# Performance work log

Hardware: AMD Instinct MI355X
Metric: run time of the kernel (lower is better)

The kernel has to match this reference:

```python
import jax, jax.numpy as jnp
import numpy as np

D = 512
EPS = 1e-5  # torch BatchNorm1d default eps


def swish(x):
    return x * jax.nn.sigmoid(x)


def batchnorm_train(x, gamma, beta):
    # BatchNorm1d in training mode: biased batch stats
    m = jnp.mean(x, axis=0)
    v = jnp.mean((x - m) ** 2, axis=0)
    return gamma * (x - m) / jnp.sqrt(v + EPS) + beta


def setup_inputs() -> dict:
    key = jax.random.key(0)
    k_fea, k_w1, k_w2, k_lerp = jax.random.split(key, 4)
    bs, P = 32768, 8192
    fea = jax.random.normal(k_fea, (bs, D), dtype=jnp.float32)
    # first P rows are the minority (positive) class
    lbl = jnp.concatenate([jnp.ones((P, 1), jnp.int32), jnp.zeros((bs - P, 1), jnp.int32)], axis=0)
    scale = 1.0 / np.sqrt(D)
    W1 = jax.random.normal(k_w1, (D, D), dtype=jnp.float32) * scale
    W2 = jax.random.normal(k_w2, (D, D), dtype=jnp.float32) * scale
    b1 = jnp.zeros((D,), jnp.float32)
    b2 = jnp.zeros((D,), jnp.float32)
    g1 = jnp.ones((D,), jnp.float32)
    g2 = jnp.ones((D,), jnp.float32)
    beta1 = jnp.zeros((D,), jnp.float32)
    beta2 = jnp.zeros((D,), jnp.float32)
    lerp_w = jax.random.uniform(k_lerp, (P, 3), dtype=jnp.float32)
    return dict(fea=fea, lbl=lbl, W1=W1, b1=b1, g1=g1, beta1=beta1,
                W2=W2, b2=b2, g2=g2, beta2=beta2, lerp_w=lerp_w, num_pos=P)


def reference(fea, lbl, W1, b1, g1, beta1, W2, b2, g2, beta2, lerp_w, num_pos):
    # fea_transform: Linear -> BN -> Swish -> Linear -> BN -> Swish
    h = swish(batchnorm_train(fea @ W1 + b1, g1, beta1))
    h = swish(batchnorm_train(h @ W2 + b2, g2, beta2))

    # SMOTE path (training mode): KNN over positive-class features
    pos_idx = jnp.nonzero(lbl[:, 0] > 0, size=num_pos)[0]  # static-size gather
    x = h[pos_idx]                                          # (P, D)
    sq = jnp.sum(x * x, axis=-1)                            # (P,)
    # negative squared pairwise distance; topk largest == nearest
    neg_dist = 2.0 * (x @ x.T) - sq[:, None] - sq[None, :]  # (P, P)
    _, idx = jax.lax.top_k(neg_dist, 3)                     # (P, 3), idx[:,0] == self

    a = x[idx[:, 0]]                                        # (P, D) anchor
    b = x[idx]                                              # (P, 3, D) neighbors
    # torch.lerp(a, b, w) = a + w * (b - a), one random w per (i, j)
    new_fea = a[:, None, :] + lerp_w[..., None] * (b - a[:, None, :])
    new_fea = new_fea.reshape(-1, D)                        # (3P, D), row-major matches i,j loop order

    fea_out = jnp.concatenate([h, new_fea], axis=0)
    lbl_out = jnp.concatenate([lbl, jnp.ones((new_fea.shape[0], 1), lbl.dtype)], axis=0)
    return fea_out, lbl_out
```

## Files before the change

### kernel.cpp

```cpp
#include <hip/hip_runtime.h>
#include <math.h>

#define NEG_INF -3.402823466e38f

typedef __attribute__((ext_vector_type(8))) short bf16x8;
typedef __attribute__((ext_vector_type(4))) float f32x4;

__device__ __forceinline__ void gload_lds16(const unsigned short* g, unsigned short* l) {
  __builtin_amdgcn_global_load_lds(
      (const __attribute__((address_space(1))) unsigned int*)g,
      (__attribute__((address_space(3))) unsigned int*)l, 16, 0, 0);
}
__device__ __forceinline__ void gload_lds16f(const float* g, float* l) {
  __builtin_amdgcn_global_load_lds(
      (const __attribute__((address_space(1))) unsigned int*)g,
      (__attribute__((address_space(3))) unsigned int*)l, 16, 0, 0);
}

__device__ __forceinline__ unsigned short f2bf(float f) {
  union { float f; unsigned int u; } a; a.f = f;
  unsigned int u = a.u;
  return (unsigned short)((u + 0x7fffu + ((u >> 16) & 1u)) >> 16);
}

__device__ __forceinline__ void split3_8(f32x4 a, f32x4 b,
                                         bf16x8& hi, bf16x8& md, bf16x8& lo) {
  union { bf16x8 v; unsigned int u[4]; } H, M, L;
  float f[8];
  f[0]=a[0]; f[1]=a[1]; f[2]=a[2]; f[3]=a[3];
  f[4]=b[0]; f[5]=b[1]; f[6]=b[2]; f[7]=b[3];
#pragma unroll
  for (int p = 0; p < 4; ++p) {
    union { float f; unsigned int u; } x0, x1, h0, h1, r0, r1, m0, m1, s0, s1;
    x0.f = f[2*p]; x1.f = f[2*p+1];
    H.u[p] = (x0.u >> 16) | (x1.u & 0xffff0000u);
    h0.u = x0.u & 0xffff0000u; h1.u = x1.u & 0xffff0000u;
    r0.f = x0.f - h0.f;        r1.f = x1.f - h1.f;
    M.u[p] = (r0.u >> 16) | (r1.u & 0xffff0000u);
    m0.u = r0.u & 0xffff0000u; m1.u = r1.u & 0xffff0000u;
    s0.f = r0.f - m0.f;        s1.f = r1.f - m1.f;
    L.u[p] = (s0.u >> 16) | (s1.u & 0xffff0000u);
  }
  hi = H.v; md = M.v; lo = L.v;
}

__global__ __launch_bounds__(256) void split_w_t3(const float* __restrict__ W,
    unsigned short* __restrict__ Th, unsigned short* __restrict__ Tm,
    unsigned short* __restrict__ Tl)
{
  __shared__ float T[64][65];
  int k0 = blockIdx.x * 64, n0 = blockIdx.y * 64;
  int tid = threadIdx.x;
  int r = tid >> 4, c4 = (tid & 15) << 2;
#pragma unroll
  for (int p = 0; p < 4; ++p) {
    int row = r + p * 16;
    float4 v = *(const float4*)&W[(size_t)(k0 + row) * 512 + n0 + c4];
    T[c4 + 0][row] = v.x; T[c4 + 1][row] = v.y;
    T[c4 + 2][row] = v.z; T[c4 + 3][row] = v.w;
  }
  __syncthreads();
  int nr = tid >> 2, kc = (tid & 3) << 4;
#pragma unroll
  for (int u = 0; u < 16; ++u) {
    union { float f; unsigned int u; } x, h, rr, m, ss;
    x.f = T[nr][kc + u];
    unsigned short hb = (unsigned short)(x.u >> 16);
    h.u = x.u & 0xffff0000u;
    rr.f = x.f - h.f;
    unsigned short mb = (unsigned short)(rr.u >> 16);
    m.u = rr.u & 0xffff0000u;
    ss.f = rr.f - m.f;
    unsigned short lb = (unsigned short)(ss.u >> 16);
    size_t o = (size_t)(n0 + nr) * 512 + k0 + kc + u;
    Th[o] = hb; Tm[o] = mb; Tl[o] = lb;
  }
}

__global__ __launch_bounds__(256, 2) void gemm_split3(
    const float* __restrict__ A, const unsigned short* __restrict__ Bth,
    const unsigned short* __restrict__ Btm, const unsigned short* __restrict__ Btl,
    const float* __restrict__ bias, float* __restrict__ C, float* __restrict__ partial)
{
  __shared__ char smem[81920];
  const int tid = threadIdx.x;
  const int w = tid >> 6, lane = tid & 63;
  const int bm = blockIdx.x * 128, bn = blockIdx.y * 128;
  const int fr = lane & 15, fg = lane >> 4;
  const int arow = tid >> 3, acb = (tid & 7) << 4;
  const int brow = tid >> 2, bcb = (tid & 3) << 4;

  f32x4 acc[2][8];
#pragma unroll
  for (int mi = 0; mi < 2; ++mi)
#pragma unroll
    for (int ni = 0; ni < 8; ++ni) acc[mi][ni] = (f32x4){0.f, 0.f, 0.f, 0.f};

  auto STAGE = [&](int buf, int ktf) {
    float* sA = (float*)(smem + buf * 40960);
    unsigned short* sBh = (unsigned short*)(smem + buf * 40960 + 16384);
    unsigned short* sBm = sBh + 4096;
    unsigned short* sBl = sBm + 4096;
#pragma unroll
    for (int p = 0; p < 4; ++p) {
      int row = arow + p * 32;
      int cb = acb ^ ((row & 7) << 4);
      gload_lds16f(&A[(size_t)(bm + row) * 512 + ktf + (cb >> 2)],
                   &sA[row * 32 + (acb >> 2)]);
    }
#pragma unroll
    for (int p = 0; p < 2; ++p) {
      int row = brow + p * 64;
      int cb = bcb ^ (((row >> 1) & 3) << 4);
      int so = row * 32 + (bcb >> 1);
      gload_lds16(&Bth[(size_t)(bn + row) * 512 + ktf + (cb >> 1)], &sBh[so]);
      gload_lds16(&Btm[(size_t)(bn + row) * 512 + ktf + (cb >> 1)], &sBm[so]);
      gload_lds16(&Btl[(size_t)(bn + row) * 512 + ktf + (cb >> 1)], &sBl[so]);
    }
  };

  STAGE(0, 0);
  __syncthreads();
  for (int it = 0; it < 16; ++it) {
    int cur = it & 1;
    if (it + 1 < 16) STAGE(cur ^ 1, (it + 1) * 32);
    float* sA = (float*)(smem + cur * 40960);
    unsigned short* sBh = (unsigned short*)(smem + cur * 40960 + 16384);
    unsigned short* sBm = sBh + 4096;
    unsigned short* sBl = sBm + 4096;
    bf16x8 ah[2], am[2], al[2];
#pragma unroll
    for (int mi = 0; mi < 2; ++mi) {
      int row = w * 32 + mi * 16 + fr;
      int swz = (row & 7) << 4;
      const char* rb = (const char*)(sA + row * 32);
      f32x4 f0 = *(const f32x4*)(rb + ((fg * 32) ^ swz));
      f32x4 f1 = *(const f32x4*)(rb + ((fg * 32 + 16) ^ swz));
      split3_8(f0, f1, ah[mi], am[mi], al[mi]);
    }
#pragma unroll
    for (int ni = 0; ni < 8; ++ni) {
      int row = ni * 16 + fr;
      int off = row * 32 + (((fg * 16) ^ (((row >> 1) & 3) << 4)) >> 1);
      bf16x8 bh  = *(const bf16x8*)&sBh[off];
      bf16x8 bmf = *(const bf16x8*)&sBm[off];
      bf16x8 blf = *(const bf16x8*)&sBl[off];
#pragma unroll
      for (int mi = 0; mi < 2; ++mi) {
        acc[mi][ni] = __builtin_amdgcn_mfma_f32_16x16x32_bf16(al[mi], bh,  acc[mi][ni], 0, 0, 0);
        acc[mi][ni] = __builtin_amdgcn_mfma_f32_16x16x32_bf16(am[mi], bmf, acc[mi][ni], 0, 0, 0);
        acc[mi][ni] = __builtin_amdgcn_mfma_f32_16x16x32_bf16(ah[mi], blf, acc[mi][ni], 0, 0, 0);
        acc[mi][ni] = __builtin_amdgcn_mfma_f32_16x16x32_bf16(am[mi], bh,  acc[mi][ni], 0, 0, 0);
        acc[mi][ni] = __builtin_amdgcn_mfma_f32_16x16x32_bf16(ah[mi], bmf, acc[mi][ni], 0, 0, 0);
        acc[mi][ni] = __builtin_amdgcn_mfma_f32_16x16x32_bf16(ah[mi], bh,  acc[mi][ni], 0, 0, 0);
      }
    }
    __syncthreads();
  }

  float ssv[8], qqv[8];
#pragma unroll
  for (int ni = 0; ni < 8; ++ni) {
    float bno = bias[bn + ni * 16 + fr];
    float s = 0.f, q = 0.f;
#pragma unroll
    for (int mi = 0; mi < 2; ++mi) {
      int row = bm + w * 32 + mi * 16 + fg * 4;
      int col = bn + ni * 16 + fr;
#pragma unroll
      for (int r = 0; r < 4; ++r) {
        float v = acc[mi][ni][r] + bno;
        C[(size_t)(row + r) * 512 + col] = v;
        s += v; q += v * v;
      }
    }
    s += __shfl_xor(s, 16); s += __shfl_xor(s, 32);
    q += __shfl_xor(q, 16); q += __shfl_xor(q, 32);
    ssv[ni] = s; qqv[ni] = q;
  }
  float* ps = (float*)smem;
  if (fg == 0) {
#pragma unroll
    for (int ni = 0; ni < 8; ++ni) {
      ps[((w * 2 + 0) * 8 + ni) * 16 + fr] = ssv[ni];
      ps[((w * 2 + 1) * 8 + ni) * 16 + fr] = qqv[ni];
    }
  }
  __syncthreads();
  if ((w & 1) == 0) {
    int p = w >> 1;
#pragma unroll
    for (int k = 0; k < 4; ++k) {
      int idx = k * 64 + lane;
      int part = idx >> 7;
      int rem = idx & 127;
      int ni = rem >> 4, fr2 = rem & 15;
      float v = ps[(((2 * p) * 2 + part) * 8 + ni) * 16 + fr2]
              + ps[(((2 * p + 1) * 2 + part) * 8 + ni) * 16 + fr2];
      int slot = blockIdx.x * 2 + p;
      partial[(size_t)(slot * 2 + part) * 512 + bn + ni * 16 + fr2] = v;
    }
  }
}

__global__ __launch_bounds__(256) void bn_reduce1(
    const float* __restrict__ partial, float* __restrict__ partial2, int nslot)
{
  int g = blockIdx.x, p = blockIdx.y;
  int per = nslot >> 4;
  int t = threadIdx.x;
#pragma unroll
  for (int cc = 0; cc < 2; ++cc) {
    int c = t + cc * 256;
    float s = 0.f;
    for (int s0 = 0; s0 < per; ++s0) {
      int slot = g * per + s0;
      s += partial[(size_t)(slot * 2 + p) * 512 + c];
    }
    partial2[(size_t)(g * 2 + p) * 512 + c] = s;
  }
}

__global__ void bn_finalize(
    const float* __restrict__ partial2, const float* __restrict__ g,
    const float* __restrict__ beta, float* __restrict__ scale,
    float* __restrict__ shift, int rows)
{
  int c = blockIdx.x * blockDim.x + threadIdx.x;
  if (c >= 512) return;
  float s = 0, s2 = 0;
  for (int b = 0; b < 16; ++b) {
    s  += partial2[(size_t)(b * 2 + 0) * 512 + c];
    s2 += partial2[(size_t)(b * 2 + 1) * 512 + c];
  }
  float m = s / rows;
  float v = s2 / rows - m * m;
  if (v < 0) v = 0;
  float sc = g[c] / sqrtf(v + 1e-5f);
  scale[c] = sc;
  shift[c] = beta[c] - m * sc;
}

__global__ void bn_swish(
    const float* __restrict__ Y, const float* __restrict__ scale,
    const float* __restrict__ shift, float* __restrict__ H, int total4)
{
  int i = blockIdx.x * blockDim.x + threadIdx.x;
  if (i >= total4) return;
  float4 y = ((const float4*)Y)[i];
  int c = (i * 4) & 511;
  float z;
  float4 o;
  z = y.x * scale[c + 0] + shift[c + 0]; o.x = z / (1.f + expf(-z));
  z = y.y * scale[c + 1] + shift[c + 1]; o.y = z / (1.f + expf(-z));
  z = y.z * scale[c + 2] + shift[c + 2]; o.z = z / (1.f + expf(-z));
  z = y.w * scale[c + 3] + shift[c + 3]; o.w = z / (1.f + expf(-z));
  ((float4*)H)[i] = o;
}

__global__ __launch_bounds__(1024) void pos_count(const int* __restrict__ lbl, int n,
                                                  int* __restrict__ cnt,
                                                  int* __restrict__ pos, int P)
{
  int b = blockIdx.x, tid = threadIdx.x;
  int i = b * 1024 + tid;
  if (i < P) pos[i] = 0;
  int pred = (i < n) && (lbl[i] > 0);
  unsigned long long m = __ballot(pred);
  __shared__ int ws[16];
  if ((tid & 63) == 0) ws[tid >> 6] = __popcll(m);
  __syncthreads();
  if (tid == 0) { int s = 0; for (int k = 0; k < 16; ++k) s += ws[k]; cnt[b] = s; }
}

__global__ void pos_prefix(int* __restrict__ cnt, int nb)
{
  if (threadIdx.x == 0) {
    int s = 0;
    for (int b = 0; b < nb; ++b) { int c = cnt[b]; cnt[b] = s; s += c; }
  }
}

__global__ __launch_bounds__(1024) void pos_scatter(const int* __restrict__ lbl, int n,
                                                    const int* __restrict__ cntp,
                                                    int* __restrict__ pos, int P)
{
  int b = blockIdx.x, tid = threadIdx.x;
  int i = b * 1024 + tid;
  int pred = (i < n) && (lbl[i] > 0);
  unsigned long long m = __ballot(pred);
  __shared__ int ws[16];
  int wid = tid >> 6, lane = tid & 63;
  if (lane == 0) ws[wid] = __popcll(m);
  __syncthreads();
  int wbase = 0;
  for (int w2 = 0; w2 < wid; ++w2) wbase += ws[w2];
  int rank = cntp[b] + wbase + __popcll(m & ((1ull << lane) - 1ull));
  if (pred && rank < P) pos[rank] = i;
}

__global__ void gather_sq(const float* __restrict__ H, const int* __restrict__ pos,
                          float* __restrict__ X, unsigned short* __restrict__ Xh,
                          float* __restrict__ sq)
{
  int r = blockIdx.x, t = threadIdx.x;
  int src = pos[r];
  float4 v = *(const float4*)&H[src * 512 + t * 4];
  *(float4*)&X[r * 512 + t * 4] = v;
  ushort4 hv;
  hv.x = f2bf(v.x); hv.y = f2bf(v.y); hv.z = f2bf(v.z); hv.w = f2bf(v.w);
  *(ushort4*)&Xh[r * 512 + t * 4] = hv;
  float s = v.x * v.x + v.y * v.y + v.z * v.z + v.w * v.w;
#pragma unroll
  for (int off = 32; off > 0; off >>= 1) s += __shfl_down(s, off);
  __shared__ float red[2];
  if ((t & 63) == 0) red[t >> 6] = s;
  __syncthreads();
  if (t == 0) sq[r] = red[0] + red[1];
}

__global__ __launch_bounds__(256, 4) void gram_sym(
    const unsigned short* __restrict__ Xh, const float* __restrict__ sq,
    float* __restrict__ p8v, int* __restrict__ p8j)
{
  __shared__ char smem[33792];
  __shared__ float sqi_l[128], sqj_l[128];
  unsigned short* Ah = (unsigned short*)smem;
  unsigned short* Bh = (unsigned short*)(smem + 16384);
  float (*dl)[64][33] = (float (*)[64][33])(void*)smem;
  float* mv = (float*)smem;
  int*   mj = (int*)(smem + 8192);

  const int tid = threadIdx.x;
  const int w = tid >> 6, lane = tid & 63;
  const int wr = w >> 1, wc = w & 1;
  const int fr = lane & 15, fg = lane >> 4;
  const int srow = tid >> 3;
  const int scb  = (tid & 7) << 4;

  int t = blockIdx.x;
  int a = (int)(64.5f - sqrtf(64.5f * 64.5f - 2.0f * (float)t));
  if (a < 0) a = 0;
  while (a > 0 && (a * (129 - a)) / 2 > t) --a;
  while (((a + 1) * (128 - a)) / 2 <= t) ++a;
  int b = a + (t - (a * (129 - a)) / 2);
  const int ai0 = a * 128, bj0 = b * 128;

  if (tid < 128) { sqi_l[tid] = sq[ai0 + tid]; sqj_l[tid] = sq[bj0 + tid]; }

  f32x4 acc[4][4];
#pragma unroll
  for (int mi = 0; mi < 4; ++mi)
#pragma unroll
    for (int ni = 0; ni < 4; ++ni) acc[mi][ni] = (f32x4){0.f, 0.f, 0.f, 0.f};

  for (int kt = 0; kt < 512; kt += 64) {
#pragma unroll
    for (int it = 0; it < 4; ++it) {
      int row = srow + it * 32;
      int cb = scb ^ ((row & 7) << 4);
      gload_lds16(&Xh[(size_t)(ai0 + row) * 512 + kt + (cb >> 1)],
                  &Ah[row * 64 + (scb >> 1)]);
      gload_lds16(&Xh[(size_t)(bj0 + row) * 512 + kt + (cb >> 1)],
                  &Bh[row * 64 + (scb >> 1)]);
    }
    __syncthreads();
#pragma unroll
    for (int ks = 0; ks < 2; ++ks) {
      bf16x8 af[4], bfr[4];
      int kb = ks * 64 + fg * 16;
#pragma unroll
      for (int mi = 0; mi < 4; ++mi) {
        int row = wr * 64 + mi * 16 + fr;
        af[mi] = *(const bf16x8*)&Ah[row * 64 + ((kb ^ ((row & 7) << 4)) >> 1)];
      }
#pragma unroll
      for (int ni = 0; ni < 4; ++ni) {
        int row = wc * 64 + ni * 16 + fr;
        bfr[ni] = *(const bf16x8*)&Bh[row * 64 + ((kb ^ ((row & 7) << 4)) >> 1)];
      }
#pragma unroll
      for (int mi = 0; mi < 4; ++mi)
#pragma unroll
        for (int ni = 0; ni < 4; ++ni)
          acc[mi][ni] = __builtin_amdgcn_mfma_f32_16x16x32_bf16(
              af[mi], bfr[ni], acc[mi][ni], 0, 0, 0);
    }
    __syncthreads();
  }

  float t8[8]; int j8[8];
#pragma unroll
  for (int q = 0; q < 8; ++q) { t8[q] = NEG_INF; j8[q] = 0x7fffffff; }

#pragma unroll
  for (int qp = 0; qp < 2; ++qp) {
#pragma unroll
    for (int qh = 0; qh < 2; ++qh) {
      int qn = qp * 2 + qh;
      float sqv = sqj_l[wc * 64 + qn * 16 + fr];
#pragma unroll
      for (int mi = 0; mi < 4; ++mi)
#pragma unroll
        for (int r = 0; r < 4; ++r)
          dl[w][mi * 16 + fg * 4 + r][qh * 16 + fr] = 2.0f * acc[mi][qn][r] - sqv;
    }
    __syncthreads();
    int jbase = bj0 + wc * 64 + qp * 32;
    for (int c = 0; c < 32; ++c) {
      float v = dl[w][lane][c];
      if (v > t8[7]) {
        t8[7] = v; j8[7] = jbase + c;
#pragma unroll
        for (int q = 7; q > 0; --q)
          if (t8[q] > t8[q - 1]) {
            float tv = t8[q]; t8[q] = t8[q - 1]; t8[q - 1] = tv;
            int tj = j8[q]; j8[q] = j8[q - 1]; j8[q - 1] = tj;
          }
      }
    }
    __syncthreads();
  }
#pragma unroll
  for (int q = 0; q < 8; ++q) {
    mv[(w * 64 + lane) * 8 + q] = t8[q];
    mj[(w * 64 + lane) * 8 + q] = j8[q];
  }
  __syncthreads();
  if ((w & 1) == 0) {
    int row = ai0 + (w >> 1) * 64 + lane;
    const float* v0 = &mv[(w * 64 + lane) * 8];
    const int*   c0 = &mj[(w * 64 + lane) * 8];
    const float* v1 = &mv[((w + 1) * 64 + lane) * 8];
    const int*   c1 = &mj[((w + 1) * 64 + lane) * 8];
    size_t ob = ((size_t)row * 64 + b) * 8;
    int h0 = 0, h1 = 0;
    for (int k = 0; k < 8; ++k) {
      float a0 = (h0 < 8) ? v0[h0] : NEG_INF;
      float a1 = (h1 < 8) ? v1[h1] : NEG_INF;
      int   b0 = (h0 < 8) ? c0[h0] : 0x7fffffff;
      int   b1 = (h1 < 8) ? c1[h1] : 0x7fffffff;
      bool take0 = (a0 > a1) || (a0 == a1 && b0 < b1);
      p8v[ob + k] = take0 ? a0 : a1;
      p8j[ob + k] = take0 ? b0 : b1;
      if (take0) ++h0; else ++h1;
    }
  }

  if (a != b) {
    __syncthreads();
#pragma unroll
    for (int q = 0; q < 8; ++q) { t8[q] = NEG_INF; j8[q] = 0x7fffffff; }
#pragma unroll
    for (int mp = 0; mp < 2; ++mp) {
#pragma unroll
      for (int mh = 0; mh < 2; ++mh) {
        int mi = mp * 2 + mh;
        f32x4 sv = *(const f32x4*)&sqi_l[wr * 64 + mi * 16 + fg * 4];
#pragma unroll
        for (int ni = 0; ni < 4; ++ni)
#pragma unroll
          for (int r = 0; r < 4; ++r)
            dl[w][ni * 16 + fr][mh * 16 + fg * 4 + r] = 2.0f * acc[mi][ni][r] - sv[r];
      }
      __syncthreads();
      int ibase = ai0 + wr * 64 + mp * 32;
      for (int c = 0; c < 32; ++c) {
        float v = dl[w][lane][c];
        if (v > t8[7]) {
          t8[7] = v; j8[7] = ibase + c;
#pragma unroll
          for (int q = 7; q > 0; --q)
            if (t8[q] > t8[q - 1]) {
              float tv = t8[q]; t8[q] = t8[q - 1]; t8[q - 1] = tv;
              int tj = j8[q]; j8[q] = j8[q - 1]; j8[q - 1] = tj;
            }
        }
      }
      __syncthreads();
    }
#pragma unroll
    for (int q = 0; q < 8; ++q) {
      mv[(w * 64 + lane) * 8 + q] = t8[q];
      mj[(w * 64 + lane) * 8 + q] = j8[q];
    }
    __syncthreads();
    if (wr == 0) {
      int row = bj0 + wc * 64 + lane;
      const float* v0 = &mv[(w * 64 + lane) * 8];
      const int*   c0 = &mj[(w * 64 + lane) * 8];
      const float* v1 = &mv[((w + 2) * 64 + lane) * 8];
      const int*   c1 = &mj[((w + 2) * 64 + lane) * 8];
      size_t ob = ((size_t)row * 64 + a) * 8;
      int h0 = 0, h1 = 0;
      for (int k = 0; k < 8; ++k) {
        float a0 = (h0 < 8) ? v0[h0] : NEG_INF;
        float a1 = (h1 < 8) ? v1[h1] : NEG_INF;
        int   b0 = (h0 < 8) ? c0[h0] : 0x7fffffff;
        int   b1 = (h1 < 8) ? c1[h1] : 0x7fffffff;
        bool take0 = (a0 > a1) || (a0 == a1 && b0 < b1);
        p8v[ob + k] = take0 ? a0 : a1;
        p8j[ob + k] = take0 ? b0 : b1;
        if (take0) ++h0; else ++h1;
      }
    }
  }
}

__global__ __launch_bounds__(256) void merge8w(const float* __restrict__ p8v,
                                               const int* __restrict__ p8j,
                                               int* __restrict__ cand, int P)
{
  int row = blockIdx.x * 4 + (threadIdx.x >> 6);
  int lane = threadIdx.x & 63;
  if (row >= P) return;
  const float* v = p8v + (size_t)row * 512 + lane * 8;
  const int* j = p8j + (size_t)row * 512 + lane * 8;
  float vv[8]; int jj[8];
#pragma unroll
  for (int q = 0; q < 8; ++q) { vv[q] = v[q]; jj[q] = j[q]; }
  for (int k = 0; k < 8; ++k) {
    float cv = vv[0]; int cj = jj[0];
#pragma unroll
    for (int off = 1; off < 64; off <<= 1) {
      float ov = __shfl_xor(cv, off);
      int oj = __shfl_xor(cj, off);
      if (ov > cv || (ov == cv && oj < cj)) { cv = ov; cj = oj; }
    }
    if (lane == 0) cand[row * 8 + k] = cj;
    if (jj[0] == cj) {
#pragma unroll
      for (int q = 0; q < 7; ++q) { vv[q] = vv[q + 1]; jj[q] = jj[q + 1]; }
      vv[7] = NEG_INF; jj[7] = 0x7fffffff;
    }
  }
}

__global__ __launch_bounds__(64) void rescore(
    const float* __restrict__ X, const float* __restrict__ sq,
    const int* __restrict__ cand, int* __restrict__ idx3)
{
  int i = blockIdx.x;
  int lane = threadIdx.x;
  f32x4 x0 = *(const f32x4*)&X[(size_t)i * 512 + lane * 8];
  f32x4 x1 = *(const f32x4*)&X[(size_t)i * 512 + lane * 8 + 4];
  float d[8]; int cj[8];
#pragma unroll
  for (int c = 0; c < 8; ++c) {
    int j = cand[i * 8 + c];
    cj[c] = j;
    f32x4 y0 = *(const f32x4*)&X[(size_t)j * 512 + lane * 8];
    f32x4 y1 = *(const f32x4*)&X[(size_t)j * 512 + lane * 8 + 4];
    float p = x0.x * y0.x + x0.y * y0.y + x0.z * y0.z + x0.w * y0.w
            + x1.x * y1.x + x1.y * y1.y + x1.z * y1.z + x1.w * y1.w;
#pragma unroll
    for (int off = 32; off > 0; off >>= 1) p += __shfl_xor(p, off);
    d[c] = 2.0f * p - sq[i] - sq[j];
  }
  if (lane == 0) {
    for (int k = 0; k < 3; ++k) {
      int b = 0;
#pragma unroll
      for (int c = 1; c < 8; ++c)
        if (d[c] > d[b] || (d[c] == d[b] && cj[c] < cj[b])) b = c;
      idx3[i * 3 + k] = cj[b];
      d[b] = NEG_INF; cj[b] = 0x7fffffff;
    }
  }
}

__global__ void make_newfea(const float* __restrict__ X, const int* __restrict__ idx3,
                            const float* __restrict__ lw, float* __restrict__ out)
{
  int r = blockIdx.x;
  int i = r / 3, k = r - i * 3;
  int ai = idx3[i * 3 + 0];
  int bi = idx3[i * 3 + k];
  float w = lw[r];
  int t = threadIdx.x;
  float4 av = *(const float4*)&X[ai * 512 + t * 4];
  float4 bv = *(const float4*)&X[bi * 512 + t * 4];
  float4 o;
  o.x = av.x + w * (bv.x - av.x);
  o.y = av.y + w * (bv.y - av.y);
  o.z = av.z + w * (bv.z - av.z);
  o.w = av.w + w * (bv.w - av.w);
  *(float4*)&out[(size_t)r * 512 + t * 4] = o;
}

__global__ void write_lbl(const int* __restrict__ lbl, float* __restrict__ out,
                          int n_in, int n_total)
{
  int i = blockIdx.x * blockDim.x + threadIdx.x;
  if (i < n_total) out[i] = (i < n_in) ? (float)lbl[i] : 1.0f;
}

extern "C" void kernel_launch(void* const* d_in, const int* in_sizes, int n_in,
                              void* d_out, int out_size, void* d_ws, size_t ws_size,
                              hipStream_t stream)
{
  const float* fea   = (const float*)d_in[0];
  const int*   lbl   = (const int*)d_in[1];
  const float* W1    = (const float*)d_in[2];
  const float* b1    = (const float*)d_in[3];
  const float* g1    = (const float*)d_in[4];
  const float* beta1 = (const float*)d_in[5];
  const float* W2    = (const float*)d_in[6];
  const float* b2    = (const float*)d_in[7];
  const float* g2    = (const float*)d_in[8];
  const float* beta2 = (const float*)d_in[9];
  const float* lerp_w = (const float*)d_in[10];

  int bs = in_sizes[0] / 512;
  int P  = in_sizes[10] / 3;
  int n_total = bs + 3 * P;

  float* out_f = (float*)d_out;
  float* Hout = out_f;
  float* newfea = out_f + (size_t)bs * 512;
  float* lbl_out = out_f + (size_t)n_total * 512;

  const size_t MB = 1024 * 1024;
  const size_t KB = 1024;
  char* ws = (char*)d_ws;
  float* Y1 = (float*)ws;
  float* X  = (float*)(ws + 64 * MB);
  unsigned short* W1h = (unsigned short*)(ws + 64 * MB);
  unsigned short* W1m = (unsigned short*)(ws + 64 * MB + 512 * KB);
  unsigned short* W1l = (unsigned short*)(ws + 64 * MB + 1024 * KB);
  unsigned short* W2h = (unsigned short*)(ws + 64 * MB + 1536 * KB);
  unsigned short* W2m = (unsigned short*)(ws + 64 * MB + 2048 * KB);
  unsigned short* W2l = (unsigned short*)(ws + 64 * MB + 2560 * KB);
  float* partial = (float*)(ws + 80 * MB);
  float* scale = (float*)(ws + 82 * MB);
  float* shiftv = scale + 512;
  float* sq = shiftv + 512;
  int* pos = (int*)(sq + 8192);
  int* idx3 = pos + 8192;
  int* cnt = idx3 + 3 * 8192;
  float* partial2 = (float*)(ws + 83 * MB);
  unsigned short* Xh = (unsigned short*)ws;
  float* p8v = (float*)(ws + 8 * MB);
  int*   p8j = (int*)(ws + 24 * MB);
  int*   cand = (int*)(ws + 40 * MB);

  dim3 wgrid(8, 8);
  split_w_t3<<<wgrid, 256, 0, stream>>>(W1, W1h, W1m, W1l);
  split_w_t3<<<wgrid, 256, 0, stream>>>(W2, W2h, W2m, W2l);

  dim3 ggrid(bs / 128, 4);
  int nslot = (bs / 128) * 2;
  dim3 rgrid(16, 2);

  gemm_split3<<<ggrid, 256, 0, stream>>>(fea, W1h, W1m, W1l, b1, Y1, partial);
  bn_reduce1<<<rgrid, 256, 0, stream>>>(partial, partial2, nslot);
  bn_finalize<<<2, 256, 0, stream>>>(partial2, g1, beta1, scale, shiftv, bs);
  bn_swish<<<(bs * 512 / 4 + 255) / 256, 256, 0, stream>>>(Y1, scale, shiftv, Y1, bs * 512 / 4);

  gemm_split3<<<ggrid, 256, 0, stream>>>(Y1, W2h, W2m, W2l, b2, Hout, partial);
  bn_reduce1<<<rgrid, 256, 0, stream>>>(partial, partial2, nslot);
  bn_finalize<<<2, 256, 0, stream>>>(partial2, g2, beta2, scale, shiftv, bs);
  bn_swish<<<(bs * 512 / 4 + 255) / 256, 256, 0, stream>>>(Hout, scale, shiftv, Hout, bs * 512 / 4);

  int nb = (bs + 1023) / 1024;
  pos_count<<<nb, 1024, 0, stream>>>(lbl, bs, cnt, pos, P);
  pos_prefix<<<1, 64, 0, stream>>>(cnt, nb);
  pos_scatter<<<nb, 1024, 0, stream>>>(lbl, bs, cnt, pos, P);
  gather_sq<<<P, 128, 0, stream>>>(Hout, pos, X, Xh, sq);

  int nbk = P / 128;
  int ntri = nbk * (nbk + 1) / 2;
  gram_sym<<<ntri, 256, 0, stream>>>(Xh, sq, p8v, p8j);
  merge8w<<<(P + 3) / 4, 256, 0, stream>>>(p8v, p8j, cand, P);
  rescore<<<P, 64, 0, stream>>>(X, sq, cand, idx3);

  make_newfea<<<3 * P, 128, 0, stream>>>(X, idx3, lerp_w, newfea);
  write_lbl<<<(n_total + 255) / 256, 256, 0, stream>>>(lbl, lbl_out, bs, n_total);
}
```

Measured before the change: 459.0 us.

## Store first-layer activations pre-split into bf16 triplets for second GEMM

The first GEMM epilogue now writes its output as three bf16 planes (hi/mid/lo) instead of fp32. The BN+swish pass works on and re-emits these planes, so the second GEMM (new gemm_presplit3) loads bf16 operands directly into LDS and skips splitting inside its K loop. make_newfea also handles three lerp rows per block and writes the anchor row without arithmetic. In exchange, the activation data moves as three 16-bit planes instead of one fp32 buffer, and the lo plane borrows the output's newfea region as scratch.

```diff
diff --git a/kernel.cpp b/kernel.cpp
--- a/kernel.cpp
+++ b/kernel.cpp
@@ -21,6 +21,20 @@
   union { float f; unsigned int u; } a; a.f = f;
   unsigned int u = a.u;
   return (unsigned short)((u + 0x7fffu + ((u >> 16) & 1u)) >> 16);
+}
+__device__ __forceinline__ float bf2f(unsigned short h) {
+  union { unsigned int u; float f; } a; a.u = ((unsigned int)h) << 16; return a.f;
+}
+
+__device__ __forceinline__ void split3_1(float v, unsigned short& h,
+                                         unsigned short& m, unsigned short& l) {
+  union { float f; unsigned int u; } x, hh, rr, mm, ss;
+  x.f = v;
+  h = (unsigned short)(x.u >> 16); hh.u = x.u & 0xffff0000u;
+  rr.f = x.f - hh.f;
+  m = (unsigned short)(rr.u >> 16); mm.u = rr.u & 0xffff0000u;
+  ss.f = rr.f - mm.f;
+  l = (unsigned short)(ss.u >> 16);
 }
 
 __device__ __forceinline__ void split3_8(f32x4 a, f32x4 b,
@@ -63,15 +77,8 @@
   int nr = tid >> 2, kc = (tid & 3) << 4;
 #pragma unroll
   for (int u = 0; u < 16; ++u) {
-    union { float f; unsigned int u; } x, h, rr, m, ss;
-    x.f = T[nr][kc + u];
-    unsigned short hb = (unsigned short)(x.u >> 16);
-    h.u = x.u & 0xffff0000u;
-    rr.f = x.f - h.f;
-    unsigned short mb = (unsigned short)(rr.u >> 16);
-    m.u = rr.u & 0xffff0000u;
-    ss.f = rr.f - m.f;
-    unsigned short lb = (unsigned short)(ss.u >> 16);
+    unsigned short hb, mb, lb;
+    split3_1(T[nr][kc + u], hb, mb, lb);
     size_t o = (size_t)(n0 + nr) * 512 + k0 + kc + u;
     Th[o] = hb; Tm[o] = mb; Tl[o] = lb;
   }
@@ -80,7 +87,9 @@
 __global__ __launch_bounds__(256, 2) void gemm_split3(
     const float* __restrict__ A, const unsigned short* __restrict__ Bth,
     const unsigned short* __restrict__ Btm, const unsigned short* __restrict__ Btl,
-    const float* __restrict__ bias, float* __restrict__ C, float* __restrict__ partial)
+    const float* __restrict__ bias,
+    unsigned short* __restrict__ Yh, unsigned short* __restrict__ Ym,
+    unsigned short* __restrict__ Yl, float* __restrict__ partial)
 {
   __shared__ char smem[81920];
   const int tid = threadIdx.x;
@@ -170,7 +179,10 @@
 #pragma unroll
       for (int r = 0; r < 4; ++r) {
         float v = acc[mi][ni][r] + bno;
-        C[(size_t)(row + r) * 512 + col] = v;
+        unsigned short hb, mb, lb;
+        split3_1(v, hb, mb, lb);
+        size_t o = (size_t)(row + r) * 512 + col;
+        Yh[o] = hb; Ym[o] = mb; Yl[o] = lb;
         s += v; q += v * v;
       }
     }
@@ -203,6 +215,116 @@
   }
 }
 
+__global__ __launch_bounds__(256, 3) void gemm_presplit3(
+    const unsigned short* __restrict__ Ah, const unsigned short* __restrict__ Am,
+    const unsigned short* __restrict__ Al,
+    const unsigned short* __restrict__ Bth, const unsigned short* __restrict__ Btm,
+    const unsigned short* __restrict__ Btl,
+    const float* __restrict__ bias, float* __restrict__ C, float* __restrict__ partial)
+{
+  __shared__ unsigned short sm[6 * 4096];
+  const int tid = threadIdx.x;
+  const int w = tid >> 6, lane = tid & 63;
+  const int bm = blockIdx.x * 128, bn = blockIdx.y * 128;
+  const int fr = lane & 15, fg = lane >> 4;
+  const int brow = tid >> 2, bcb = (tid & 3) << 4;
+
+  f32x4 acc[2][8];
+#pragma unroll
+  for (int mi = 0; mi < 2; ++mi)
+#pragma unroll
+    for (int ni = 0; ni < 8; ++ni) acc[mi][ni] = (f32x4){0.f, 0.f, 0.f, 0.f};
+
+  for (int kt = 0; kt < 512; kt += 32) {
+#pragma unroll
+    for (int p = 0; p < 2; ++p) {
+      int row = brow + p * 64;
+      int cb = bcb ^ (((row >> 1) & 3) << 4);
+      int so = row * 32 + (bcb >> 1);
+      size_t ga = (size_t)(bm + row) * 512 + kt + (cb >> 1);
+      size_t gb = (size_t)(bn + row) * 512 + kt + (cb >> 1);
+      gload_lds16(&Ah[ga],  &sm[0 * 4096 + so]);
+      gload_lds16(&Am[ga],  &sm[1 * 4096 + so]);
+      gload_lds16(&Al[ga],  &sm[2 * 4096 + so]);
+      gload_lds16(&Bth[gb], &sm[3 * 4096 + so]);
+      gload_lds16(&Btm[gb], &sm[4 * 4096 + so]);
+      gload_lds16(&Btl[gb], &sm[5 * 4096 + so]);
+    }
+    __syncthreads();
+    bf16x8 ah[2], am[2], al[2];
+#pragma unroll
+    for (int mi = 0; mi < 2; ++mi) {
+      int row = w * 32 + mi * 16 + fr;
+      int off = row * 32 + (((fg * 16) ^ (((row >> 1) & 3) << 4)) >> 1);
+      ah[mi] = *(const bf16x8*)&sm[0 * 4096 + off];
+      am[mi] = *(const bf16x8*)&sm[1 * 4096 + off];
+      al[mi] = *(const bf16x8*)&sm[2 * 4096 + off];
+    }
+#pragma unroll
+    for (int ni = 0; ni < 8; ++ni) {
+      int row = ni * 16 + fr;
+      int off = row * 32 + (((fg * 16) ^ (((row >> 1) & 3) << 4)) >> 1);
+      bf16x8 bh  = *(const bf16x8*)&sm[3 * 4096 + off];
+      bf16x8 bmf = *(const bf16x8*)&sm[4 * 4096 + off];
+      bf16x8 blf = *(const bf16x8*)&sm[5 * 4096 + off];
+#pragma unroll
+      for (int mi = 0; mi < 2; ++mi) {
+        acc[mi][ni] = __builtin_amdgcn_mfma_f32_16x16x32_bf16(al[mi], bh,  acc[mi][ni], 0, 0, 0);
+        acc[mi][ni] = __builtin_amdgcn_mfma_f32_16x16x32_bf16(am[mi], bmf, acc[mi][ni], 0, 0, 0);
+        acc[mi][ni] = __builtin_amdgcn_mfma_f32_16x16x32_bf16(ah[mi], blf, acc[mi][ni], 0, 0, 0);
+        acc[mi][ni] = __builtin_amdgcn_mfma_f32_16x16x32_bf16(am[mi], bh,  acc[mi][ni], 0, 0, 0);
+        acc[mi][ni] = __builtin_amdgcn_mfma_f32_16x16x32_bf16(ah[mi], bmf, acc[mi][ni], 0, 0, 0);
+        acc[mi][ni] = __builtin_amdgcn_mfma_f32_16x16x32_bf16(ah[mi], bh,  acc[mi][ni], 0, 0, 0);
+      }
+    }
+    __syncthreads();
+  }
+
+  float ssv[8], qqv[8];
+#pragma unroll
+  for (int ni = 0; ni < 8; ++ni) {
+    float bno = bias[bn + ni * 16 + fr];
+    float s = 0.f, q = 0.f;
+#pragma unroll
+    for (int mi = 0; mi < 2; ++mi) {
+      int row = bm + w * 32 + mi * 16 + fg * 4;
+      int col = bn + ni * 16 + fr;
+#pragma unroll
+      for (int r = 0; r < 4; ++r) {
+        float v = acc[mi][ni][r] + bno;
+        C[(size_t)(row + r) * 512 + col] = v;
+        s += v; q += v * v;
+      }
+    }
+    s += __shfl_xor(s, 16); s += __shfl_xor(s, 32);
+    q += __shfl_xor(q, 16); q += __shfl_xor(q, 32);
+    ssv[ni] = s; qqv[ni] = q;
+  }
+  float* ps = (float*)sm;
+  if (fg == 0) {
+#pragma unroll
+    for (int ni = 0; ni < 8; ++ni) {
+      ps[((w * 2 + 0) * 8 + ni) * 16 + fr] = ssv[ni];
+      ps[((w * 2 + 1) * 8 + ni) * 16 + fr] = qqv[ni];
+    }
+  }
+  __syncthreads();
+  if ((w & 1) == 0) {
+    int p = w >> 1;
+#pragma unroll
+    for (int k = 0; k < 4; ++k) {
+      int idx = k * 64 + lane;
+      int part = idx >> 7;
+      int rem = idx & 127;
+      int ni = rem >> 4, fr2 = rem & 15;
+      float v = ps[(((2 * p) * 2 + part) * 8 + ni) * 16 + fr2]
+              + ps[(((2 * p + 1) * 2 + part) * 8 + ni) * 16 + fr2];
+      int slot = blockIdx.x * 2 + p;
+      partial[(size_t)(slot * 2 + part) * 512 + bn + ni * 16 + fr2] = v;
+    }
+  }
+}
+
 __global__ __launch_bounds__(256) void bn_reduce1(
     const float* __restrict__ partial, float* __restrict__ partial2, int nslot)
 {
@@ -239,6 +361,38 @@
   float sc = g[c] / sqrtf(v + 1e-5f);
   scale[c] = sc;
   shift[c] = beta[c] - m * sc;
+}
+
+__global__ void bn_swish_split3(
+    unsigned short* __restrict__ Ph, unsigned short* __restrict__ Pm,
+    unsigned short* __restrict__ Pl,
+    const float* __restrict__ scale, const float* __restrict__ shift, int total8)
+{
+  int i = blockIdx.x * blockDim.x + threadIdx.x;
+  if (i >= total8) return;
+  size_t base = (size_t)i * 8;
+  ushort4 h0 = *(ushort4*)&Ph[base], h1 = *(ushort4*)&Ph[base + 4];
+  ushort4 m0 = *(ushort4*)&Pm[base], m1 = *(ushort4*)&Pm[base + 4];
+  ushort4 l0 = *(ushort4*)&Pl[base], l1 = *(ushort4*)&Pl[base + 4];
+  int c = (int)(base & 511);
+  unsigned short hs[8] = {h0.x, h0.y, h0.z, h0.w, h1.x, h1.y, h1.z, h1.w};
+  unsigned short ms[8] = {m0.x, m0.y, m0.z, m0.w, m1.x, m1.y, m1.z, m1.w};
+  unsigned short ls[8] = {l0.x, l0.y, l0.z, l0.w, l1.x, l1.y, l1.z, l1.w};
+  f32x4 va, vb;
+#pragma unroll
+  for (int u = 0; u < 8; ++u) {
+    float v = (bf2f(hs[u]) + bf2f(ms[u])) + bf2f(ls[u]);
+    float z = v * scale[c + u] + shift[c + u];
+    float sw = z / (1.f + expf(-z));
+    if (u < 4) va[u] = sw; else vb[u - 4] = sw;
+  }
+  bf16x8 H, M, L;
+  split3_8(va, vb, H, M, L);
+  union { bf16x8 v; ushort4 q[2]; } uH, uM, uL;
+  uH.v = H; uM.v = M; uL.v = L;
+  *(ushort4*)&Ph[base] = uH.q[0]; *(ushort4*)&Ph[base + 4] = uH.q[1];
+  *(ushort4*)&Pm[base] = uM.q[0]; *(ushort4*)&Pm[base + 4] = uM.q[1];
+  *(ushort4*)&Pl[base] = uL.q[0]; *(ushort4*)&Pl[base + 4] = uL.q[1];
 }
 
 __global__ void bn_swish(
@@ -572,20 +726,23 @@
 __global__ void make_newfea(const float* __restrict__ X, const int* __restrict__ idx3,
                             const float* __restrict__ lw, float* __restrict__ out)
 {
-  int r = blockIdx.x;
-  int i = r / 3, k = r - i * 3;
+  int i = blockIdx.x;
+  int t = threadIdx.x;
   int ai = idx3[i * 3 + 0];
-  int bi = idx3[i * 3 + k];
-  float w = lw[r];
-  int t = threadIdx.x;
-  float4 av = *(const float4*)&X[ai * 512 + t * 4];
-  float4 bv = *(const float4*)&X[bi * 512 + t * 4];
-  float4 o;
-  o.x = av.x + w * (bv.x - av.x);
-  o.y = av.y + w * (bv.y - av.y);
-  o.z = av.z + w * (bv.z - av.z);
-  o.w = av.w + w * (bv.w - av.w);
-  *(float4*)&out[(size_t)r * 512 + t * 4] = o;
+  float4 av = *(const float4*)&X[(size_t)ai * 512 + t * 4];
+  *(float4*)&out[(size_t)(i * 3) * 512 + t * 4] = av;
+#pragma unroll
+  for (int k = 1; k < 3; ++k) {
+    int bi = idx3[i * 3 + k];
+    float w = lw[i * 3 + k];
+    float4 bv = *(const float4*)&X[(size_t)bi * 512 + t * 4];
+    float4 o;
+    o.x = av.x + w * (bv.x - av.x);
+    o.y = av.y + w * (bv.y - av.y);
+    o.z = av.z + w * (bv.z - av.z);
+    o.w = av.w + w * (bv.w - av.w);
+    *(float4*)&out[(size_t)(i * 3 + k) * 512 + t * 4] = o;
+  }
 }
 
 __global__ void write_lbl(const int* __restrict__ lbl, float* __restrict__ out,
@@ -623,7 +780,9 @@
   const size_t MB = 1024 * 1024;
   const size_t KB = 1024;
   char* ws = (char*)d_ws;
-  float* Y1 = (float*)ws;
+  unsigned short* A1h = (unsigned short*)ws;
+  unsigned short* A1m = (unsigned short*)(ws + 32 * MB);
+  unsigned short* A1l = (unsigned short*)newfea;
   float* X  = (float*)(ws + 64 * MB);
   unsigned short* W1h = (unsigned short*)(ws + 64 * MB);
   unsigned short* W1m = (unsigned short*)(ws + 64 * MB + 512 * KB);
@@ -651,13 +810,14 @@
   dim3 ggrid(bs / 128, 4);
   int nslot = (bs / 128) * 2;
   dim3 rgrid(16, 2);
-
-  gemm_split3<<<ggrid, 256, 0, stream>>>(fea, W1h, W1m, W1l, b1, Y1, partial);
+  int total8 = bs * 512 / 8;
+
+  gemm_split3<<<ggrid, 256, 0, stream>>>(fea, W1h, W1m, W1l, b1, A1h, A1m, A1l, partial);
   bn_reduce1<<<rgrid, 256, 0, stream>>>(partial, partial2, nslot);
   bn_finalize<<<2, 256, 0, stream>>>(partial2, g1, beta1, scale, shiftv, bs);
-  bn_swish<<<(bs * 512 / 4 + 255) / 256, 256, 0, stream>>>(Y1, scale, shiftv, Y1, bs * 512 / 4);
-
-  gemm_split3<<<ggrid, 256, 0, stream>>>(Y1, W2h, W2m, W2l, b2, Hout, partial);
+  bn_swish_split3<<<(total8 + 255) / 256, 256, 0, stream>>>(A1h, A1m, A1l, scale, shiftv, total8);
+
+  gemm_presplit3<<<ggrid, 256, 0, stream>>>(A1h, A1m, A1l, W2h, W2m, W2l, b2, Hout, partial);
   bn_reduce1<<<rgrid, 256, 0, stream>>>(partial, partial2, nslot);
   bn_finalize<<<2, 256, 0, stream>>>(partial2, g2, beta2, scale, shiftv, bs);
   bn_swish<<<(bs * 512 / 4 + 255) / 256, 256, 0, stream>>>(Hout, scale, shiftv, Hout, bs * 512 / 4);
@@ -674,6 +834,6 @@
   merge8w<<<(P + 3) / 4, 256, 0, stream>>>(p8v, p8j, cand, P);
   rescore<<<P, 64, 0, stream>>>(X, sq, cand, idx3);
 
-  make_newfea<<<3 * P, 128, 0, stream>>>(X, idx3, lerp_w, newfea);
+  make_newfea<<<P, 128, 0, stream>>>(X, idx3, lerp_w, newfea);
   write_lbl<<<(n_total + 255) / 256, 256, 0, stream>>>(lbl, lbl_out, bs, n_total);
 }
```

Measured after the change: 494.2 us. 1.08x slower.
